# Kernel optimization log

Hardware: AMD Instinct MI355X
Metric: run time of the kernel (lower is better)

## Reference

```python
import jax, jax.numpy as jnp
import numpy as np

N, E, D, ED, H, MAXDEG = 50000, 800000, 128, 64, 8, 512
C = D // H


def _ln(x, g, b, eps=1e-5):
    m = jnp.mean(x, axis=-1, keepdims=True)
    v = jnp.var(x, axis=-1, keepdims=True)
    return (x - m) * jax.lax.rsqrt(v + eps) * g + b


def setup_inputs() -> dict:
    key = jax.random.key(0)
    ks = jax.random.split(key, 16)
    nrm = lambda k, s: jax.random.normal(k, s, jnp.float32) * 0.02
    return {
        "x": jax.random.normal(ks[0], (N, D), jnp.float32),
        "edge_index": jax.random.randint(ks[1], (2, E), 0, N, dtype=jnp.int32),
        "edge_attr": jax.random.normal(ks[2], (E, ED), jnp.float32),
        "deg_emb": nrm(ks[3], (MAXDEG, D)),
        "ln_g": jnp.ones((D,), jnp.float32), "ln_b": jnp.zeros((D,), jnp.float32),
        "Wq": nrm(ks[4], (D, D)), "bq": jnp.zeros((D,), jnp.float32),
        "Wk": nrm(ks[5], (D, D)), "bk": jnp.zeros((D,), jnp.float32),
        "Wv": nrm(ks[6], (D, D)), "bv": jnp.zeros((D,), jnp.float32),
        "We": nrm(ks[7], (ED, D)), "be": jnp.zeros((D,), jnp.float32),
        "Wskip": nrm(ks[8], (D, D)), "bskip": jnp.zeros((D,), jnp.float32),
        "W1": nrm(ks[9], (D, 4 * D)), "b1": jnp.zeros((4 * D,), jnp.float32),
        "W2": nrm(ks[10], (4 * D, D)), "b2": jnp.zeros((D,), jnp.float32),
        "eu_ln_g": jnp.ones((D,), jnp.float32), "eu_ln_b": jnp.zeros((D,), jnp.float32),
        "Wm": nrm(ks[11], (2 * D + ED, 2 * ED)), "bm": jnp.zeros((2 * ED,), jnp.float32),
        "eln_g": jnp.ones((ED,), jnp.float32), "eln_b": jnp.zeros((ED,), jnp.float32),
    }


def reference(x, edge_index, edge_attr, deg_emb, ln_g, ln_b, Wq, bq, Wk, bk, Wv, bv,
              We, be, Wskip, bskip, W1, b1, W2, b2, eu_ln_g, eu_ln_b, Wm, bm, eln_g, eln_b):
    n = x.shape[0]
    src, dst = edge_index[0], edge_index[1]

    # degree embedding: out-degree via scatter-add on src, clamped
    deg = jax.ops.segment_sum(jnp.ones_like(src), src, num_segments=n)
    x_in = x + deg_emb[jnp.clip(deg, 0, MAXDEG - 1)]

    # pre-norm (same LayerNorm module used for attn and ffn branches)
    h = _ln(x_in, ln_g, ln_b)

    # TransformerConv: per-edge gather -> score -> segment softmax -> scatter
    q = (h @ Wq + bq).reshape(n, H, C)
    k = (h @ Wk + bk).reshape(n, H, C)
    v = (h @ Wv + bv).reshape(n, H, C)
    e = (edge_attr @ We + be).reshape(-1, H, C)  # [E,H,C]

    ke = k[src] + e
    alpha = jnp.sum(q[dst] * ke, axis=-1) / jnp.sqrt(jnp.float32(C))  # [E,H]
    amax = jax.ops.segment_max(alpha, dst, num_segments=n)
    amax = jnp.where(jnp.isfinite(amax), amax, 0.0)
    ex = jnp.exp(alpha - amax[dst])
    denom = jax.ops.segment_sum(ex, dst, num_segments=n)
    w = ex / (denom[dst] + 1e-16)  # [E,H]

    msg = (v[src] + e) * w[:, :, None]
    out = jax.ops.segment_sum(msg, dst, num_segments=n).reshape(n, D)
    h_attn = out + h @ Wskip + bskip  # root skip on normed input

    x_attn = x_in + h_attn

    # FFN with pre-norm (norm_type == 'layer')
    hf = _ln(x_attn, ln_g, ln_b)
    ffn = jax.nn.gelu(hf @ W1 + b1, approximate=False) @ W2 + b2
    x_new = x_attn + ffn

    # EdgeUpdate: gated residual MLP on gathered node pairs
    xn = _ln(x_new, eu_ln_g, eu_ln_b)
    m = jnp.concatenate([xn[src], xn[dst], edge_attr], axis=-1)  # [E, 2D+ED]
    raw = jax.nn.relu(m @ Wm + bm)
    delta, gate = jnp.split(raw, 2, axis=-1)
    ea_new = _ln(edge_attr + jax.nn.sigmoid(gate) * delta, eln_g, eln_b)

    return x_new, ea_new
```

## Files before the change

kernel.cpp:

```cpp
#include <hip/hip_runtime.h>
#include <hip/hip_bf16.h>
#include <math.h>

constexpr int N_NODES = 50000;
constexpr int N_EDGES = 800000;
constexpr int D  = 128;
constexpr int ED = 64;

typedef __attribute__((ext_vector_type(8))) short short8;
typedef __attribute__((ext_vector_type(4))) float f32x4;

static __device__ __forceinline__ float allsum64(float v){
#pragma unroll
  for(int off=32; off>=1; off>>=1) v += __shfl_xor(v, off, 64);
  return v;
}

static __device__ __forceinline__ short bfs(float f){
  __hip_bfloat16 h = __float2bfloat16(f);
  return *reinterpret_cast<short*>(&h);
}
static __device__ __forceinline__ float bf2f(short s){
  __hip_bfloat16 h = *reinterpret_cast<__hip_bfloat16*>(&s);
  return __bfloat162float(h);
}
static __device__ __forceinline__ float lo16(int w){ return bf2f((short)(w & 0xffff)); }
static __device__ __forceinline__ float hi16(int w){ return bf2f((short)(((unsigned)w) >> 16)); }

template<typename T> __device__ __forceinline__ T cvt_out(float v);
template<> __device__ __forceinline__ float cvt_out<float>(float v){ return v; }
template<> __device__ __forceinline__ __hip_bfloat16 cvt_out<__hip_bfloat16>(float v){ return __float2bfloat16(v); }

__global__ void k_deg(const int* __restrict__ src, const int* __restrict__ dst,
                      int* __restrict__ deg, int* __restrict__ hist){
  int i = blockIdx.x*256 + threadIdx.x;
  if(i < N_EDGES){
    atomicAdd(&deg[src[i]], 1);
    atomicAdd(&hist[dst[i]], 1);
  }
}

__global__ __launch_bounds__(1024) void k_scan(const int* __restrict__ hist,
                                               int* __restrict__ rows,
                                               int* __restrict__ cursor){
  __shared__ int part[1024];
  const int t = threadIdx.x;
  const int CH = (N_NODES + 1023) / 1024;
  int base = t*CH;
  int s = 0;
  for(int i=0;i<CH;i++){ int idx=base+i; if(idx<N_NODES) s += hist[idx]; }
  part[t] = s; __syncthreads();
  for(int off=1; off<1024; off<<=1){
    int v = (t>=off) ? part[t-off] : 0;
    __syncthreads();
    part[t] += v;
    __syncthreads();
  }
  int run = part[t] - s;
  for(int i=0;i<CH;i++){
    int idx=base+i;
    if(idx<N_NODES){ rows[idx]=run; cursor[idx]=run; run += hist[idx]; }
  }
  if(t==1023) rows[N_NODES] = run;
}

__global__ void k_scatter(const int* __restrict__ src, const int* __restrict__ dst,
                          int* __restrict__ cursor,
                          int* __restrict__ perm, int* __restrict__ ssrc){
  int e = blockIdx.x*256 + threadIdx.x;
  if(e < N_EDGES){
    int p = atomicAdd(&cursor[dst[e]], 1);
    perm[p] = e;
    ssrc[p] = src[e];
  }
}

__global__ __launch_bounds__(256) void k_node_prep(
    const float* __restrict__ x, const int* __restrict__ deg,
    const float* __restrict__ deg_emb, const float* __restrict__ g,
    const float* __restrict__ b, float* __restrict__ xin, short* __restrict__ h){
  int node = blockIdx.x*4 + (threadIdx.x>>6);
  int lane = threadIdx.x & 63;
  if(node >= N_NODES) return;
  int dg = deg[node]; dg = dg > 511 ? 511 : dg;
  const float* xr = x + (size_t)node*D;
  const float* er = deg_emb + (size_t)dg*D;
  float a0 = xr[lane]    + er[lane];
  float a1 = xr[lane+64] + er[lane+64];
  float* xo = xin + (size_t)node*D;
  xo[lane] = a0; xo[lane+64] = a1;
  float s  = allsum64(a0+a1);
  float s2 = allsum64(a0*a0 + a1*a1);
  float mean = s * (1.f/128.f);
  float var  = s2 * (1.f/128.f) - mean*mean;
  float rs = rsqrtf(var + 1e-5f);
  h[(size_t)node*D + lane]    = bfs((a0-mean)*rs*g[lane]    + b[lane]);
  h[(size_t)node*D + lane+64] = bfs((a1-mean)*rs*g[lane+64] + b[lane+64]);
}

__global__ void k_pack(const float* __restrict__ Wq, const float* __restrict__ Wk,
                       const float* __restrict__ Wv, const float* __restrict__ Ws,
                       const float* __restrict__ bq, const float* __restrict__ bk,
                       const float* __restrict__ bv, const float* __restrict__ bs,
                       float* __restrict__ Wcat, float* __restrict__ bcat){
  int idx = blockIdx.x*256 + threadIdx.x;
  if(idx < D*4*D){
    int i = idx >> 9, j = idx & 511;
    int sel = j >> 7, jj = j & 127;
    const float* W = sel==0?Wq: sel==1?Wk: sel==2?Wv:Ws;
    Wcat[idx] = W[i*D + jj];
  } else if(idx < D*4*D + 4*D){
    int j = idx - D*4*D;
    int sel = j>>7, jj = j&127;
    const float* B = sel==0?bq: sel==1?bk: sel==2?bv:bs;
    bcat[j] = B[jj];
  }
}

__global__ void k_packWN(const float* __restrict__ W, short* __restrict__ out,
                         int K, int Nfull){
  int idx = blockIdx.x*256 + threadIdx.x;
  if(idx >= K*Nfull) return;
  int KC = K >> 5;
  int j  = idx & 7;
  int l  = (idx>>3) & 63;
  int cf = (idx>>9) & 7;
  int rest = idx >> 12;
  int kc = rest % KC;
  int nb = rest / KC;
  int k = kc*32 + ((l>>4)<<3) + j;
  int n = nb*128 + (cf<<4) + (l&15);
  out[idx] = bfs(W[(size_t)k*Nfull + n]);
}

template<int ACT, int OMAP, typename OutT, typename AT>
__global__ __launch_bounds__(256) void k_gemm_mfma(
    const AT* __restrict__ A, const short* __restrict__ Wp,
    const float* __restrict__ bias,
    OutT* __restrict__ C, int M, int K, int Nfull){
  const int tid = threadIdx.x, lane = tid & 63, wid = tid >> 6;
  const int l16 = lane & 15, lg = lane >> 4;
  const int KC = K >> 5;
  const size_t rowb = (size_t)blockIdx.x*64 + wid*16;
  const int nb = blockIdx.y;
  size_t arow = rowb + l16; if(arow >= (size_t)M) arow = M-1;
  f32x4 acc[8] = {};
  const short8* Bg = ((const short8*)Wp) + (size_t)nb*KC*512 + lane;
  for(int kc=0; kc<KC; kc++){
    short8 a;
    if constexpr (sizeof(AT)==4){
      const float* ap = (const float*)A + arow*K + kc*32 + lg*8;
      float4 f0 = *(const float4*)ap;
      float4 f1 = *(const float4*)(ap+4);
      a[0]=bfs(f0.x); a[1]=bfs(f0.y); a[2]=bfs(f0.z); a[3]=bfs(f0.w);
      a[4]=bfs(f1.x); a[5]=bfs(f1.y); a[6]=bfs(f1.z); a[7]=bfs(f1.w);
    } else {
      a = *(const short8*)((const short*)A + arow*K + kc*32 + lg*8);
    }
#pragma unroll
    for(int cf=0;cf<8;cf++){
      short8 b = Bg[(kc*8+cf)*64];
      acc[cf] = __builtin_amdgcn_mfma_f32_16x16x32_bf16(a, b, acc[cf], 0, 0, 0);
    }
  }
#pragma unroll
  for(int cf=0;cf<8;cf++){
    int cIn = cf*16 + l16;
    int col = nb*128 + cIn;
    float bb = bias[col];
    int stCol;
    if(OMAP == 1){
      if(nb==0)      stCol = 2*(cIn&63) + (cIn>>6);
      else if(nb==1) stCol = 128 + 4*(cIn&63) + (cIn>>6);
      else if(nb==2) stCol = 128 + 4*(cIn&63) + 2 + (cIn>>6);
      else           stCol = 384 + 2*(cIn&63) + (cIn>>6);
    } else stCol = col;
#pragma unroll
    for(int r=0;r<4;r++){
      size_t ro = rowb + lg*4 + r;
      if(ro < (size_t)M){
        float v = acc[cf][r] + bb;
        if(ACT == 1) v = v * 0.5f * (1.f + erff(v * 0.70710678118f));
        C[ro*Nfull + stCol] = cvt_out<OutT>(v);
      }
    }
  }
}

__global__ __launch_bounds__(256) void k_ffn2_ln(
    const short* __restrict__ A, const short* __restrict__ Wp,
    const float* __restrict__ bias, const float* __restrict__ Src,
    const float* __restrict__ g, const float* __restrict__ bv,
    float* __restrict__ xnew, short* __restrict__ xn, int M){
  const int tid = threadIdx.x, lane = tid & 63, wid = tid >> 6;
  const int l16 = lane & 15, lg = lane >> 4;
  const size_t rowb = (size_t)blockIdx.x*64 + wid*16;
  size_t arow = rowb + l16; if(arow >= (size_t)M) arow = M-1;
  f32x4 acc[8] = {};
  const short8* Bg = ((const short8*)Wp) + lane;
  for(int kc=0; kc<16; kc++){
    short8 a = *(const short8*)(A + arow*512 + kc*32 + lg*8);
#pragma unroll
    for(int cf=0;cf<8;cf++){
      short8 b = Bg[(kc*8+cf)*64];
      acc[cf] = __builtin_amdgcn_mfma_f32_16x16x32_bf16(a, b, acc[cf], 0, 0, 0);
    }
  }
  float vals[8][4];
#pragma unroll
  for(int cf=0;cf<8;cf++){
    int col = cf*16 + l16;
    float bb = bias[col];
#pragma unroll
    for(int r=0;r<4;r++){
      size_t ro = rowb + lg*4 + r; if(ro >= (size_t)M) ro = M-1;
      vals[cf][r] = acc[cf][r] + bb + Src[ro*128 + col];
    }
  }
#pragma unroll
  for(int r=0;r<4;r++){
    float s1 = 0.f, s2 = 0.f;
#pragma unroll
    for(int cf=0;cf<8;cf++){ s1 += vals[cf][r]; s2 += vals[cf][r]*vals[cf][r]; }
#pragma unroll
    for(int off=1; off<16; off<<=1){
      s1 += __shfl_xor(s1, off, 64);
      s2 += __shfl_xor(s2, off, 64);
    }
    float mean = s1 * (1.f/128.f);
    float var  = s2 * (1.f/128.f) - mean*mean;
    float rs = rsqrtf(var + 1e-5f);
    size_t ro = rowb + lg*4 + r;
    if(ro < (size_t)M){
#pragma unroll
      for(int cf=0;cf<8;cf++){
        int col = cf*16 + l16;
        xnew[ro*128 + col] = vals[cf][r];
        xn[ro*128 + col] = bfs((vals[cf][r]-mean)*rs*g[col] + bv[col]);
      }
    }
  }
}

__global__ __launch_bounds__(256) void k_eproj_sorted(
    const float* __restrict__ eattr, const int* __restrict__ perm,
    const short* __restrict__ Wep, const float* __restrict__ be,
    short* __restrict__ out){
  const int tid = threadIdx.x, lane = tid & 63, wid = tid >> 6;
  const int l16 = lane & 15, lg = lane >> 4;
  const size_t row = (size_t)blockIdx.x*64 + wid*16;
  const int pe = perm[row + l16];
  f32x4 acc[8] = {};
  const short8* Bg = ((const short8*)Wep) + lane;
  const float* ga = eattr + (size_t)pe*64;
#pragma unroll
  for(int kc=0;kc<2;kc++){
    int cb = kc*32 + lg*8;
    float4 f0 = *(const float4*)(ga + cb);
    float4 f1 = *(const float4*)(ga + cb + 4);
    short8 a;
    a[0]=bfs(f0.x); a[1]=bfs(f0.y); a[2]=bfs(f0.z); a[3]=bfs(f0.w);
    a[4]=bfs(f1.x); a[5]=bfs(f1.y); a[6]=bfs(f1.z); a[7]=bfs(f1.w);
#pragma unroll
    for(int cf=0;cf<8;cf++){
      short8 b = Bg[(kc*8+cf)*64];
      acc[cf] = __builtin_amdgcn_mfma_f32_16x16x32_bf16(a, b, acc[cf], 0, 0, 0);
    }
  }
#pragma unroll
  for(int cf=0;cf<8;cf++){
    int col = cf*16 + l16;
    int stCol = 2*(col&63) + (col>>6);
    float bb = be[col];
#pragma unroll
    for(int r=0;r<4;r++){
      size_t ro = row + lg*4 + r;
      out[ro*128 + stCol] = bfs(acc[cf][r] + bb);
    }
  }
}

__global__ __launch_bounds__(256) void k_attn_fused3(
    const int* __restrict__ ssrc, const int* __restrict__ rows,
    const short* __restrict__ qk, const short* __restrict__ es,
    const float* __restrict__ xin, const float* __restrict__ g,
    const float* __restrict__ b,
    float* __restrict__ xattn, short* __restrict__ hf){
  int n = blockIdx.x*4 + (threadIdx.x>>6);
  int lane = threadIdx.x & 63;
  if(n >= N_NODES) return;
  const short* qrow = qk + (size_t)n*512;
  int qw = *(const int*)(qrow + 2*lane);
  float q0 = lo16(qw), q1 = hi16(qw);
  float m0=-INFINITY, m1=-INFINITY;
  float den0=0.f, den1=0.f, acc0=0.f, acc1=0.f;
  int i = rows[n];
  const int i1 = rows[n+1];

  for(; i+2 <= i1; i += 2){
    int sA = ssrc[i], sB = ssrc[i+1];
    int ewA = *(const int*)(es + (size_t)i*128 + 2*lane);
    int ewB = *(const int*)(es + (size_t)(i+1)*128 + 2*lane);
    int2 kvA = *(const int2*)(qk + (size_t)sA*512 + 128 + 4*lane);
    int2 kvB = *(const int2*)(qk + (size_t)sB*512 + 128 + 4*lane);
    float eA0=lo16(ewA), eA1=hi16(ewA);
    float eB0=lo16(ewB), eB1=hi16(ewB);
    float pA0 = q0*(lo16(kvA.x)+eA0), pA1 = q1*(hi16(kvA.x)+eA1);
    float pB0 = q0*(lo16(kvB.x)+eB0), pB1 = q1*(hi16(kvB.x)+eB1);
#pragma unroll
    for(int off=1; off<16; off<<=1){
      pA0 += __shfl_xor(pA0,off,64); pA1 += __shfl_xor(pA1,off,64);
      pB0 += __shfl_xor(pB0,off,64); pB1 += __shfl_xor(pB1,off,64);
    }
    {
      float a0 = pA0*0.25f, a1 = pA1*0.25f;
      float v0 = lo16(kvA.y)+eA0, v1 = hi16(kvA.y)+eA1;
      float mn0 = fmaxf(m0,a0), mn1 = fmaxf(m1,a1);
      float sc0 = __expf(m0-mn0), sc1 = __expf(m1-mn1);
      float ex0 = __expf(a0-mn0), ex1 = __expf(a1-mn1);
      den0 = den0*sc0 + ex0;       den1 = den1*sc1 + ex1;
      acc0 = acc0*sc0 + ex0*v0;    acc1 = acc1*sc1 + ex1*v1;
      m0 = mn0; m1 = mn1;
    }
    {
      float a0 = pB0*0.25f, a1 = pB1*0.25f;
      float v0 = lo16(kvB.y)+eB0, v1 = hi16(kvB.y)+eB1;
      float mn0 = fmaxf(m0,a0), mn1 = fmaxf(m1,a1);
      float sc0 = __expf(m0-mn0), sc1 = __expf(m1-mn1);
      float ex0 = __expf(a0-mn0), ex1 = __expf(a1-mn1);
      den0 = den0*sc0 + ex0;       den1 = den1*sc1 + ex1;
      acc0 = acc0*sc0 + ex0*v0;    acc1 = acc1*sc1 + ex1*v1;
      m0 = mn0; m1 = mn1;
    }
  }
  if(i < i1){
    int sA = ssrc[i];
    int ewA = *(const int*)(es + (size_t)i*128 + 2*lane);
    int2 kvA = *(const int2*)(qk + (size_t)sA*512 + 128 + 4*lane);
    float eA0=lo16(ewA), eA1=hi16(ewA);
    float pA0 = q0*(lo16(kvA.x)+eA0), pA1 = q1*(hi16(kvA.x)+eA1);
#pragma unroll
    for(int off=1; off<16; off<<=1){
      pA0 += __shfl_xor(pA0,off,64); pA1 += __shfl_xor(pA1,off,64);
    }
    float a0 = pA0*0.25f, a1 = pA1*0.25f;
    float v0 = lo16(kvA.y)+eA0, v1 = hi16(kvA.y)+eA1;
    float mn0 = fmaxf(m0,a0), mn1 = fmaxf(m1,a1);
    float sc0 = __expf(m0-mn0), sc1 = __expf(m1-mn1);
    float ex0 = __expf(a0-mn0), ex1 = __expf(a1-mn1);
    den0 = den0*sc0 + ex0;       den1 = den1*sc1 + ex1;
    acc0 = acc0*sc0 + ex0*v0;    acc1 = acc1*sc1 + ex1*v1;
    m0 = mn0; m1 = mn1;
  }

  float o0 = acc0/(den0+1e-16f);
  float o1 = acc1/(den1+1e-16f);
  int sw = *(const int*)(qrow + 384 + 2*lane);
  size_t base = (size_t)n*128;
  float a0 = xin[base+lane]    + o0 + lo16(sw);
  float a1 = xin[base+lane+64] + o1 + hi16(sw);
  xattn[base+lane] = a0; xattn[base+lane+64] = a1;
  float s  = allsum64(a0+a1);
  float s2 = allsum64(a0*a0 + a1*a1);
  float mean = s * (1.f/128.f);
  float var  = s2 * (1.f/128.f) - mean*mean;
  float rs = rsqrtf(var + 1e-5f);
  hf[base+lane]    = bfs((a0-mean)*rs*g[lane]    + b[lane]);
  hf[base+lane+64] = bfs((a1-mean)*rs*g[lane+64] + b[lane+64]);
}

__global__ __launch_bounds__(256) void k_edge_mfma5(
    const int* __restrict__ src, const int* __restrict__ dst,
    const short* __restrict__ xnb, const float* __restrict__ ea,
    const short* __restrict__ Wmp, const float* __restrict__ bm,
    const float* __restrict__ eg, const float* __restrict__ ebv,
    float* __restrict__ out){
  const int tid = threadIdx.x, lane = tid & 63, wid = tid >> 6;
  const int l16 = lane & 15, lg = lane >> 4;
  const size_t e0 = (size_t)blockIdx.x*128 + wid*32;
  const int ko = lg*8;
  int sI[2], dI[2];
  sI[0] = src[e0+l16];    dI[0] = dst[e0+l16];
  sI[1] = src[e0+16+l16]; dI[1] = dst[e0+16+l16];
  f32x4 acc[8][2] = {};
  const short8* Bg = ((const short8*)Wmp) + lane;

  auto load_a = [&](int kc, short8* a){
#pragma unroll
    for(int mi=0;mi<2;mi++){
      if(kc < 8){
        int node = (kc < 4) ? sI[mi] : dI[mi];
        a[mi] = *(const short8*)(xnb + (size_t)node*128 + (kc&3)*32 + ko);
      } else {
        const float* ap = ea + (e0 + mi*16 + l16)*64 + (kc-8)*32 + ko;
        float4 f0 = *(const float4*)ap;
        float4 f1 = *(const float4*)(ap+4);
        a[mi][0]=bfs(f0.x); a[mi][1]=bfs(f0.y); a[mi][2]=bfs(f0.z); a[mi][3]=bfs(f0.w);
        a[mi][4]=bfs(f1.x); a[mi][5]=bfs(f1.y); a[mi][6]=bfs(f1.z); a[mi][7]=bfs(f1.w);
      }
    }
  };

  short8 aC[2], aN[2];
  load_a(0, aC);
#pragma unroll
  for(int kc=0; kc<10; kc++){
    if(kc < 9) load_a(kc+1, aN);
#pragma unroll
    for(int cf=0;cf<8;cf++){
      short8 b = Bg[(kc*8+cf)*64];
      acc[cf][0] = __builtin_amdgcn_mfma_f32_16x16x32_bf16(aC[0], b, acc[cf][0], 0, 0, 0);
      acc[cf][1] = __builtin_amdgcn_mfma_f32_16x16x32_bf16(aC[1], b, acc[cf][1], 0, 0, 0);
    }
    aC[0] = aN[0]; aC[1] = aN[1];
  }

  float bmd[4], bmg[4], egc[4], ebc[4];
#pragma unroll
  for(int cf=0;cf<4;cf++){
    int col = cf*16 + l16;
    bmd[cf] = bm[col];
    bmg[cf] = bm[64+col];
    egc[cf] = eg[col];
    ebc[cf] = ebv[col];
  }
#pragma unroll
  for(int mi=0;mi<2;mi++){
#pragma unroll
    for(int r=0;r<4;r++){
      size_t erow = e0 + mi*16 + lg*4 + r;
      float u[4];
      float s1 = 0.f, s2 = 0.f;
#pragma unroll
      for(int cf=0;cf<4;cf++){
        float dlt = fmaxf(0.f, acc[cf][mi][r]   + bmd[cf]);
        float gt  = fmaxf(0.f, acc[cf+4][mi][r] + bmg[cf]);
        float uu = ea[erow*64 + cf*16 + l16] + dlt / (1.f + expf(-gt));
        u[cf] = uu; s1 += uu; s2 += uu*uu;
      }
#pragma unroll
      for(int off=1; off<16; off<<=1){
        s1 += __shfl_xor(s1, off, 64);
        s2 += __shfl_xor(s2, off, 64);
      }
      float mean = s1 * (1.f/64.f);
      float var  = s2 * (1.f/64.f) - mean*mean;
      float rs = rsqrtf(var + 1e-5f);
#pragma unroll
      for(int cf=0;cf<4;cf++)
        out[erow*64 + cf*16 + l16] = (u[cf]-mean)*rs*egc[cf] + ebc[cf];
    }
  }
}

extern "C" void kernel_launch(void* const* d_in, const int* in_sizes, int n_in,
                              void* d_out, int out_size, void* d_ws, size_t ws_size,
                              hipStream_t stream){
  const float* x       = (const float*)d_in[0];
  const int*   eidx    = (const int*)d_in[1];
  const float* eattr   = (const float*)d_in[2];
  const float* deg_emb = (const float*)d_in[3];
  const float* ln_g = (const float*)d_in[4];
  const float* ln_b = (const float*)d_in[5];
  const float* Wq = (const float*)d_in[6];  const float* bq = (const float*)d_in[7];
  const float* Wk = (const float*)d_in[8];  const float* bk = (const float*)d_in[9];
  const float* Wv = (const float*)d_in[10]; const float* bv = (const float*)d_in[11];
  const float* We = (const float*)d_in[12]; const float* be = (const float*)d_in[13];
  const float* Ws = (const float*)d_in[14]; const float* bs = (const float*)d_in[15];
  const float* W1 = (const float*)d_in[16]; const float* b1 = (const float*)d_in[17];
  const float* W2 = (const float*)d_in[18]; const float* b2 = (const float*)d_in[19];
  const float* eug = (const float*)d_in[20]; const float* eub = (const float*)d_in[21];
  const float* Wm = (const float*)d_in[22]; const float* bm = (const float*)d_in[23];
  const float* eg = (const float*)d_in[24]; const float* eb = (const float*)d_in[25];
  (void)in_sizes; (void)n_in; (void)out_size; (void)ws_size;

  const int* src = eidx;
  const int* dst = eidx + N_EDGES;

  float* ws = (float*)d_ws;
  size_t o = 0;
  auto alloc = [&](size_t n){ size_t r = o; o += (n + 63) & ~(size_t)63; return r; };
  size_t o_deg   = alloc(N_NODES);
  size_t o_hist  = alloc(N_NODES);
  size_t zero_f  = o;
  size_t o_rows  = alloc(N_NODES+1);
  size_t o_cur   = alloc(N_NODES);
  size_t o_perm  = alloc(N_EDGES);
  size_t o_ssrc  = alloc(N_EDGES);
  size_t o_attn  = alloc((size_t)N_NODES*D);
  size_t o_xin   = alloc((size_t)N_NODES*D);
  size_t o_h     = alloc((size_t)N_NODES*D/2);
  size_t o_qkv16 = alloc((size_t)N_NODES*256);
  size_t o_wcat  = alloc((size_t)D*4*D);
  size_t o_bcat  = alloc(4*D);
  size_t o_wqp   = alloc((size_t)128*512/2);
  size_t o_w1p   = alloc((size_t)128*512/2);
  size_t o_w2p   = alloc((size_t)512*128/2);
  size_t o_wmp   = alloc((size_t)320*128/2);
  size_t o_wep   = alloc((size_t)64*128/2);

  float* xnew_out = (float*)d_out;
  float* ea_out   = xnew_out + (size_t)N_NODES*D;
  short* es = (short*)ea_out;

  hipMemsetAsync(d_ws, 0, zero_f*sizeof(float), stream);

  k_deg<<<(N_EDGES+255)/256, 256, 0, stream>>>(src, dst, (int*)(ws+o_deg),
                                               (int*)(ws+o_hist));
  k_scan<<<1, 1024, 0, stream>>>((int*)(ws+o_hist), (int*)(ws+o_rows),
                                 (int*)(ws+o_cur));
  k_scatter<<<(N_EDGES+255)/256, 256, 0, stream>>>(src, dst, (int*)(ws+o_cur),
                                                   (int*)(ws+o_perm),
                                                   (int*)(ws+o_ssrc));
  k_node_prep<<<N_NODES/4, 256, 0, stream>>>(x, (int*)(ws+o_deg), deg_emb, ln_g, ln_b,
                                             ws+o_xin, (short*)(ws+o_h));
  k_pack<<<(D*4*D + 4*D + 255)/256, 256, 0, stream>>>(Wq,Wk,Wv,Ws, bq,bk,bv,bs,
                                                      ws+o_wcat, ws+o_bcat);
  k_packWN<<<256, 256, 0, stream>>>(ws+o_wcat, (short*)(ws+o_wqp), 128, 512);
  k_packWN<<<256, 256, 0, stream>>>(W1, (short*)(ws+o_w1p), 128, 512);
  k_packWN<<<256, 256, 0, stream>>>(W2, (short*)(ws+o_w2p), 512, 128);
  k_packWN<<<160, 256, 0, stream>>>(Wm, (short*)(ws+o_wmp), 320, 128);
  k_packWN<<<32,  256, 0, stream>>>(We, (short*)(ws+o_wep), 64, 128);
  {
    dim3 g((N_NODES+63)/64, 4);
    k_gemm_mfma<0,1,__hip_bfloat16,short><<<g,256,0,stream>>>(
        (const short*)(ws+o_h), (const short*)(ws+o_wqp), ws+o_bcat,
        (__hip_bfloat16*)(ws+o_qkv16), N_NODES, 128, 512);
  }
  k_eproj_sorted<<<N_EDGES/64, 256, 0, stream>>>(eattr, (const int*)(ws+o_perm),
                                                 (const short*)(ws+o_wep), be, es);
  k_attn_fused3<<<(N_NODES+3)/4, 256, 0, stream>>>((const int*)(ws+o_ssrc),
                                                   (int*)(ws+o_rows),
                                                   (const short*)(ws+o_qkv16), es,
                                                   ws+o_xin, ln_g, ln_b,
                                                   ws+o_attn, (short*)(ws+o_h));
  {
    dim3 g((N_NODES+63)/64, 4);
    k_gemm_mfma<1,0,__hip_bfloat16,short><<<g,256,0,stream>>>(
        (const short*)(ws+o_h), (const short*)(ws+o_w1p), b1,
        (__hip_bfloat16*)(ws+o_qkv16), N_NODES, 128, 512);
  }
  {
    dim3 g((N_NODES+63)/64);
    k_ffn2_ln<<<g,256,0,stream>>>(
        (const short*)(ws+o_qkv16), (const short*)(ws+o_w2p), b2, ws+o_attn,
        eug, eub, xnew_out, (short*)(ws+o_xin), N_NODES);
  }
  k_edge_mfma5<<<N_EDGES/128, 256, 0, stream>>>(src, dst, (const short*)(ws+o_xin),
                                                eattr, (const short*)(ws+o_wmp), bm,
                                                eg, eb, ea_out);
}
```

Measured before the change: 948.7 us.

## Precompute per-node edge-MLP projections to shrink per-edge GEMM

The edge update MLP is split algebraically: xn@Wm[0:128] and xn@Wm[128:256] are computed once per node (50k rows) in a new GEMM, stored in bf16 with an interleaved column layout. The per-edge kernel then only multiplies edge_attr by the last 64 rows of Wm and adds gathered per-node partial sums. This cuts per-edge MFMA work from K=320 to K=64 and replaces two 128-wide gathers per edge with two 128-wide gathers of precomputed results. In exchange it adds an extra node GEMM and intermediate buffer, and the bf16 rounding of the partial products changes numerics slightly.

```diff
diff --git a/kernel.cpp b/kernel.cpp
--- a/kernel.cpp
+++ b/kernel.cpp
@@ -131,6 +131,19 @@
   int k = kc*32 + ((l>>4)<<3) + j;
   int n = nb*128 + (cf<<4) + (l&15);
   out[idx] = bfs(W[(size_t)k*Nfull + n]);
+}
+
+__global__ void k_packWm12(const float* __restrict__ Wm, short* __restrict__ out){
+  int idx = blockIdx.x*256 + threadIdx.x;
+  if(idx >= 256*128) return;
+  int j  = idx & 7;
+  int l  = (idx>>3) & 63;
+  int cf = (idx>>9) & 7;
+  int rest = idx >> 12;
+  int kc = rest & 3, nb = rest >> 2;
+  int k = kc*32 + ((l>>4)<<3) + j;
+  int n = (cf<<4) + (l&15);
+  out[idx] = bfs(Wm[(size_t)(nb*128 + k)*128 + n]);
 }
 
 template<int ACT, int OMAP, typename OutT, typename AT>
@@ -174,6 +187,8 @@
       else if(nb==1) stCol = 128 + 4*(cIn&63) + (cIn>>6);
       else if(nb==2) stCol = 128 + 4*(cIn&63) + 2 + (cIn>>6);
       else           stCol = 384 + 2*(cIn&63) + (cIn>>6);
+    } else if(OMAP == 2){
+      stCol = nb*128 + (cIn&15)*8 + (cIn>>4);
     } else stCol = col;
 #pragma unroll
     for(int r=0;r<4;r++){
@@ -369,50 +384,50 @@
   hf[base+lane+64] = bfs((a1-mean)*rs*g[lane+64] + b[lane+64]);
 }
 
-__global__ __launch_bounds__(256) void k_edge_mfma5(
+__global__ __launch_bounds__(256) void k_edge_mfma6(
     const int* __restrict__ src, const int* __restrict__ dst,
-    const short* __restrict__ xnb, const float* __restrict__ ea,
-    const short* __restrict__ Wmp, const float* __restrict__ bm,
+    const short* __restrict__ P12, const float* __restrict__ ea,
+    const short* __restrict__ Wmep, const float* __restrict__ bm,
     const float* __restrict__ eg, const float* __restrict__ ebv,
     float* __restrict__ out){
   const int tid = threadIdx.x, lane = tid & 63, wid = tid >> 6;
   const int l16 = lane & 15, lg = lane >> 4;
   const size_t e0 = (size_t)blockIdx.x*128 + wid*32;
   const int ko = lg*8;
-  int sI[2], dI[2];
-  sI[0] = src[e0+l16];    dI[0] = dst[e0+l16];
-  sI[1] = src[e0+16+l16]; dI[1] = dst[e0+16+l16];
   f32x4 acc[8][2] = {};
-  const short8* Bg = ((const short8*)Wmp) + lane;
-
-  auto load_a = [&](int kc, short8* a){
+  const short8* Bg = ((const short8*)Wmep) + lane;
+
+#pragma unroll
+  for(int kc=0; kc<2; kc++){
+    short8 a[2];
 #pragma unroll
     for(int mi=0;mi<2;mi++){
-      if(kc < 8){
-        int node = (kc < 4) ? sI[mi] : dI[mi];
-        a[mi] = *(const short8*)(xnb + (size_t)node*128 + (kc&3)*32 + ko);
-      } else {
-        const float* ap = ea + (e0 + mi*16 + l16)*64 + (kc-8)*32 + ko;
-        float4 f0 = *(const float4*)ap;
-        float4 f1 = *(const float4*)(ap+4);
-        a[mi][0]=bfs(f0.x); a[mi][1]=bfs(f0.y); a[mi][2]=bfs(f0.z); a[mi][3]=bfs(f0.w);
-        a[mi][4]=bfs(f1.x); a[mi][5]=bfs(f1.y); a[mi][6]=bfs(f1.z); a[mi][7]=bfs(f1.w);
-      }
-    }
-  };
-
-  short8 aC[2], aN[2];
-  load_a(0, aC);
-#pragma unroll
-  for(int kc=0; kc<10; kc++){
-    if(kc < 9) load_a(kc+1, aN);
+      const float* ap = ea + (e0 + mi*16 + l16)*64 + kc*32 + ko;
+      float4 f0 = *(const float4*)ap;
+      float4 f1 = *(const float4*)(ap+4);
+      a[mi][0]=bfs(f0.x); a[mi][1]=bfs(f0.y); a[mi][2]=bfs(f0.z); a[mi][3]=bfs(f0.w);
+      a[mi][4]=bfs(f1.x); a[mi][5]=bfs(f1.y); a[mi][6]=bfs(f1.z); a[mi][7]=bfs(f1.w);
+    }
 #pragma unroll
     for(int cf=0;cf<8;cf++){
       short8 b = Bg[(kc*8+cf)*64];
-      acc[cf][0] = __builtin_amdgcn_mfma_f32_16x16x32_bf16(aC[0], b, acc[cf][0], 0, 0, 0);
-      acc[cf][1] = __builtin_amdgcn_mfma_f32_16x16x32_bf16(aC[1], b, acc[cf][1], 0, 0, 0);
-    }
-    aC[0] = aN[0]; aC[1] = aN[1];
+      acc[cf][0] = __builtin_amdgcn_mfma_f32_16x16x32_bf16(a[0], b, acc[cf][0], 0, 0, 0);
+      acc[cf][1] = __builtin_amdgcn_mfma_f32_16x16x32_bf16(a[1], b, acc[cf][1], 0, 0, 0);
+    }
+  }
+
+#pragma unroll
+  for(int mi=0;mi<2;mi++){
+#pragma unroll
+    for(int r=0;r<4;r++){
+      size_t erow = e0 + mi*16 + lg*4 + r;
+      int sE = src[erow], dE = dst[erow];
+      short8 p1 = *(const short8*)(P12 + (size_t)sE*256 + l16*8);
+      short8 p2 = *(const short8*)(P12 + (size_t)dE*256 + 128 + l16*8);
+#pragma unroll
+      for(int cf=0;cf<8;cf++)
+        acc[cf][mi][r] += bf2f(p1[cf]) + bf2f(p2[cf]);
+    }
   }
 
   float bmd[4], bmg[4], egc[4], ebc[4];
@@ -482,6 +497,7 @@
   auto alloc = [&](size_t n){ size_t r = o; o += (n + 63) & ~(size_t)63; return r; };
   size_t o_deg   = alloc(N_NODES);
   size_t o_hist  = alloc(N_NODES);
+  size_t o_zb    = alloc(256);
   size_t zero_f  = o;
   size_t o_rows  = alloc(N_NODES+1);
   size_t o_cur   = alloc(N_NODES);
@@ -491,12 +507,14 @@
   size_t o_xin   = alloc((size_t)N_NODES*D);
   size_t o_h     = alloc((size_t)N_NODES*D/2);
   size_t o_qkv16 = alloc((size_t)N_NODES*256);
+  size_t o_p12   = alloc((size_t)N_NODES*128);
   size_t o_wcat  = alloc((size_t)D*4*D);
   size_t o_bcat  = alloc(4*D);
   size_t o_wqp   = alloc((size_t)128*512/2);
   size_t o_w1p   = alloc((size_t)128*512/2);
   size_t o_w2p   = alloc((size_t)512*128/2);
-  size_t o_wmp   = alloc((size_t)320*128/2);
+  size_t o_wm12  = alloc((size_t)256*128/2);
+  size_t o_wmep  = alloc((size_t)64*128/2);
   size_t o_wep   = alloc((size_t)64*128/2);
 
   float* xnew_out = (float*)d_out;
@@ -519,7 +537,8 @@
   k_packWN<<<256, 256, 0, stream>>>(ws+o_wcat, (short*)(ws+o_wqp), 128, 512);
   k_packWN<<<256, 256, 0, stream>>>(W1, (short*)(ws+o_w1p), 128, 512);
   k_packWN<<<256, 256, 0, stream>>>(W2, (short*)(ws+o_w2p), 512, 128);
-  k_packWN<<<160, 256, 0, stream>>>(Wm, (short*)(ws+o_wmp), 320, 128);
+  k_packWm12<<<128, 256, 0, stream>>>(Wm, (short*)(ws+o_wm12));
+  k_packWN<<<32,  256, 0, stream>>>(Wm + 256*128, (short*)(ws+o_wmep), 64, 128);
   k_packWN<<<32,  256, 0, stream>>>(We, (short*)(ws+o_wep), 64, 128);
   {
     dim3 g((N_NODES+63)/64, 4);
@@ -546,7 +565,13 @@
         (const short*)(ws+o_qkv16), (const short*)(ws+o_w2p), b2, ws+o_attn,
         eug, eub, xnew_out, (short*)(ws+o_xin), N_NODES);
   }
-  k_edge_mfma5<<<N_EDGES/128, 256, 0, stream>>>(src, dst, (const short*)(ws+o_xin),
-                                                eattr, (const short*)(ws+o_wmp), bm,
+  {
+    dim3 g((N_NODES+63)/64, 2);
+    k_gemm_mfma<0,2,__hip_bfloat16,short><<<g,256,0,stream>>>(
+        (const short*)(ws+o_xin), (const short*)(ws+o_wm12), ws+o_zb,
+        (__hip_bfloat16*)(ws+o_p12), N_NODES, 128, 256);
+  }
+  k_edge_mfma6<<<N_EDGES/128, 256, 0, stream>>>(src, dst, (const short*)(ws+o_p12),
+                                                eattr, (const short*)(ws+o_wmep), bm,
                                                 eg, eb, ea_out);
 }
```

Measured after the change: 859.9 us. 1.1x faster.
